# Optimization experiments

Measured on AMD Instinct MI355X. Metric: run time of the kernel, lower is better.

Reference implementation:

```python
import jax, jax.numpy as jnp
import numpy as np

N = 8192
D_IN = 512
D_OUT = 512


def setup_inputs() -> dict:
    key = jax.random.key(0)
    k1, k2, k3, k4 = jax.random.split(key, 4)
    x = jax.random.normal(k1, (N, D_IN), dtype=jnp.float32)
    adj = jax.random.uniform(k2, (N, N), dtype=jnp.float32)
    # nn.Linear params: weight (out, in), bias (out,)
    bound = 1.0 / np.sqrt(D_IN)
    W = jax.random.uniform(k3, (D_OUT, D_IN), minval=-bound, maxval=bound, dtype=jnp.float32)
    b = jax.random.uniform(k4, (D_OUT,), minval=-bound, maxval=bound, dtype=jnp.float32)
    return {"x": x, "adj": adj, "W": W, "b": b}


def reference(x, adj, W, b):
    # Symmetric normalization: D^-1/2 (A + I) D^-1/2.
    # Original uses diag-matmuls; broadcast scaling is the identical math
    # without the O(n^3) diagonal GEMMs.
    a = adj + jnp.eye(adj.shape[0], dtype=adj.dtype)
    d = jnp.sum(a, axis=1) ** -0.5  # (N,)
    a_norm = d[:, None] * a * d[None, :]
    support = a_norm @ x                      # (N, D_IN)
    out = support @ W.T + b                   # (N, D_OUT)
    out = jax.nn.relu(out)
    # dropout: identity in eval/reference mode
    return out
```

## Files before the change

kernel.cpp:

```cpp
#include <hip/hip_runtime.h>
#include <stdint.h>

typedef __bf16 bf16_t;
typedef __bf16 bf16x8 __attribute__((ext_vector_type(8)));
typedef __bf16 bf16x4v __attribute__((ext_vector_type(4)));
typedef float f32x4 __attribute__((ext_vector_type(4)));

#define AS_GLOBAL __attribute__((address_space(1)))
#define AS_LDS    __attribute__((address_space(3)))

static constexpr int NN   = 8192;
static constexpr int DIN  = 512;
static constexpr int DOUT = 512;
static constexpr int SPLITK = 4;

__device__ __forceinline__ void async_cp16(const bf16_t* g, bf16_t* l) {
  __builtin_amdgcn_global_load_lds((AS_GLOBAL unsigned int*)g,
                                   (AS_LDS unsigned int*)l, 16, 0, 0);
}

__global__ __launch_bounds__(256) void k_rowsum_convert(
    const float* __restrict__ adj, bf16_t* __restrict__ adjb,
    float* __restrict__ d) {
  const int row = blockIdx.x;
  const int t = threadIdx.x;
  const float4* rf4 = (const float4*)(adj + (size_t)row * NN);
  bf16_t* outp = adjb + (size_t)row * NN;
  float sum = 0.f;
#pragma unroll
  for (int c = 0; c < 8; ++c) {
    int f4i = c * 256 + t;
    float4 a = rf4[f4i];
    sum += a.x + a.y + a.z + a.w;
    bf16x4v o;
    o[0] = (bf16_t)a.x; o[1] = (bf16_t)a.y; o[2] = (bf16_t)a.z; o[3] = (bf16_t)a.w;
    *(bf16x4v*)(outp + f4i * 4) = o;
  }
#pragma unroll
  for (int off = 32; off > 0; off >>= 1) sum += __shfl_down(sum, off);
  __shared__ float red[4];
  if ((t & 63) == 0) red[t >> 6] = sum;
  __syncthreads();
  if (t == 0) {
    float s = red[0] + red[1] + red[2] + red[3] + 1.0f;
    d[row] = rsqrtf(s);
  }
}

__global__ __launch_bounds__(256) void k_make_xsT(
    const float* __restrict__ x, const float* __restrict__ d,
    bf16_t* __restrict__ xsT) {
  __shared__ bf16_t T[64][72];
  const int t = threadIdx.x;
  const int k0 = blockIdx.x * 64, j0 = blockIdx.y * 64;
#pragma unroll
  for (int it = 0; it < 4; ++it) {
    int idx = it * 256 + t;
    int r = idx >> 4, c = idx & 15;
    float4 v = *(const float4*)(x + (size_t)(k0 + r) * DIN + j0 + c * 4);
    float s = d[k0 + r];
    T[r][c * 4 + 0] = (bf16_t)(v.x * s);
    T[r][c * 4 + 1] = (bf16_t)(v.y * s);
    T[r][c * 4 + 2] = (bf16_t)(v.z * s);
    T[r][c * 4 + 3] = (bf16_t)(v.w * s);
  }
  __syncthreads();
#pragma unroll
  for (int it = 0; it < 2; ++it) {
    int idx = it * 256 + t;
    int j = idx >> 3, kb = idx & 7;
    bf16x8 o;
#pragma unroll
    for (int e = 0; e < 8; ++e) o[e] = T[kb * 8 + e][j];
    *(bf16x8*)(xsT + (size_t)(j0 + j) * NN + k0 + kb * 8) = o;
  }
}

__global__ __launch_bounds__(256) void k_convert_w(
    const float* __restrict__ W, bf16_t* __restrict__ Wb) {
  int idx = blockIdx.x * 256 + threadIdx.x;
  float4 v = *(const float4*)(W + (size_t)idx * 4);
  bf16x4v o;
  o[0] = (bf16_t)v.x; o[1] = (bf16_t)v.y; o[2] = (bf16_t)v.z; o[3] = (bf16_t)v.w;
  *(bf16x4v*)(Wb + (size_t)idx * 4) = o;
}

__device__ __forceinline__ void gemm_tile_128x128(
    const bf16_t* __restrict__ A, const bf16_t* __restrict__ B,
    int lda, int ldb, int m0, int n0, int kStart, int kEnd,
    bf16_t* As, bf16_t* Bs, f32x4 acc[4][4]) {
  const int t = threadIdx.x;
  const int lane = t & 63;
  const int wid = t >> 6;
  const int wm = wid >> 1, wn = wid & 1;
  const int lanelo = lane & 15, quad = lane >> 4;

  const int swz = (t & 7) ^ ((t >> 3) & 7);
  const bf16_t* gA = A + (size_t)(m0 + (t >> 3)) * lda + swz * 8 + kStart;
  const bf16_t* gB = B + (size_t)(n0 + (t >> 3)) * ldb + swz * 8 + kStart;
  bf16_t* lA = As + t * 8;
  bf16_t* lB = Bs + t * 8;

  const int xorc = lanelo & 7;

  for (int k0 = kStart; k0 < kEnd; k0 += 64) {
#pragma unroll
    for (int i = 0; i < 4; ++i) {
      async_cp16(gA + (size_t)(i * 32) * lda, lA + i * 2048);
      async_cp16(gB + (size_t)(i * 32) * ldb, lB + i * 2048);
    }
    gA += 64; gB += 64;
    __syncthreads();
#pragma unroll
    for (int kk = 0; kk < 2; ++kk) {
      const int pchunk = ((kk * 4 + quad) ^ xorc) * 8;
      bf16x8 av[4], bv[4];
#pragma unroll
      for (int f = 0; f < 4; ++f) {
        av[f] = *(const bf16x8*)(As + (wm * 64 + f * 16 + lanelo) * 64 + pchunk);
        bv[f] = *(const bf16x8*)(Bs + (wn * 64 + f * 16 + lanelo) * 64 + pchunk);
      }
#pragma unroll
      for (int fm = 0; fm < 4; ++fm)
#pragma unroll
        for (int fn = 0; fn < 4; ++fn)
          acc[fm][fn] = __builtin_amdgcn_mfma_f32_16x16x32_bf16(
              av[fm], bv[fn], acc[fm][fn], 0, 0, 0);
    }
    __syncthreads();
  }
}

__global__ __launch_bounds__(256) void k_gemm1(
    const bf16_t* __restrict__ adjb, const bf16_t* __restrict__ xsT,
    float* __restrict__ part) {
  __shared__ bf16_t As[128 * 64];
  __shared__ bf16_t Bs[128 * 64];
  f32x4 acc[4][4];
  const f32x4 fzero = {0.f, 0.f, 0.f, 0.f};
#pragma unroll
  for (int a = 0; a < 4; ++a)
#pragma unroll
    for (int b = 0; b < 4; ++b) acc[a][b] = fzero;

  const int m0 = blockIdx.x * 128, n0 = blockIdx.y * 128;
  const int kc = blockIdx.z;
  const int kChunk = NN / SPLITK;
  gemm_tile_128x128(adjb, xsT, NN, NN, m0, n0, kc * kChunk, (kc + 1) * kChunk,
                    As, Bs, acc);

  const int t = threadIdx.x;
  const int lane = t & 63, wid = t >> 6;
  const int wm = wid >> 1, wn = wid & 1;
  const int lanelo = lane & 15, quad = lane >> 4;
  float* outp = part + (size_t)kc * NN * DIN;
#pragma unroll
  for (int fm = 0; fm < 4; ++fm)
#pragma unroll
    for (int fn = 0; fn < 4; ++fn) {
      int gc = n0 + wn * 64 + fn * 16 + lanelo;
#pragma unroll
      for (int r = 0; r < 4; ++r) {
        int gr = m0 + wm * 64 + fm * 16 + quad * 4 + r;
        outp[(size_t)gr * DIN + gc] = acc[fm][fn][r];
      }
    }
}

__global__ __launch_bounds__(256) void k_combine(
    const float* __restrict__ part, const float* __restrict__ d,
    const float* __restrict__ x, bf16_t* __restrict__ supB) {
  int idx = blockIdx.x * 256 + threadIdx.x;
  int i = idx >> 7;
  float4 p = *(const float4*)(part + (size_t)idx * 4);
#pragma unroll
  for (int kc = 1; kc < SPLITK; ++kc) {
    float4 q = *(const float4*)(part + (size_t)kc * NN * DIN + (size_t)idx * 4);
    p.x += q.x; p.y += q.y; p.z += q.z; p.w += q.w;
  }
  float4 xv = *(const float4*)(x + (size_t)idx * 4);
  float di = d[i];
  float dii = di * di;
  bf16x4v o;
  o[0] = (bf16_t)(di * p.x + dii * xv.x);
  o[1] = (bf16_t)(di * p.y + dii * xv.y);
  o[2] = (bf16_t)(di * p.z + dii * xv.z);
  o[3] = (bf16_t)(di * p.w + dii * xv.w);
  *(bf16x4v*)(supB + (size_t)idx * 4) = o;
}

__global__ __launch_bounds__(256) void k_gemm2(
    const bf16_t* __restrict__ supB, const bf16_t* __restrict__ Wb,
    const float* __restrict__ bias, float* __restrict__ outp) {
  __shared__ bf16_t As[128 * 64];
  __shared__ bf16_t Bs[128 * 64];
  f32x4 acc[4][4];
  const f32x4 fzero = {0.f, 0.f, 0.f, 0.f};
#pragma unroll
  for (int a = 0; a < 4; ++a)
#pragma unroll
    for (int b = 0; b < 4; ++b) acc[a][b] = fzero;

  const int m0 = blockIdx.x * 128, n0 = blockIdx.y * 128;
  gemm_tile_128x128(supB, Wb, DIN, DIN, m0, n0, 0, DIN, As, Bs, acc);

  const int t = threadIdx.x;
  const int lane = t & 63, wid = t >> 6;
  const int wm = wid >> 1, wn = wid & 1;
  const int lanelo = lane & 15, quad = lane >> 4;
#pragma unroll
  for (int fn = 0; fn < 4; ++fn) {
    int gc = n0 + wn * 64 + fn * 16 + lanelo;
    float bb = bias[gc];
#pragma unroll
    for (int fm = 0; fm < 4; ++fm)
#pragma unroll
      for (int r = 0; r < 4; ++r) {
        int gr = m0 + wm * 64 + fm * 16 + quad * 4 + r;
        float v = acc[fm][fn][r] + bb;
        outp[(size_t)gr * DOUT + gc] = v > 0.f ? v : 0.f;
      }
  }
}

extern "C" void kernel_launch(void* const* d_in, const int* in_sizes, int n_in,
                              void* d_out, int out_size, void* d_ws, size_t ws_size,
                              hipStream_t stream) {
  const float* x   = (const float*)d_in[0];
  const float* adj = (const float*)d_in[1];
  const float* W   = (const float*)d_in[2];
  const float* b   = (const float*)d_in[3];
  float* out = (float*)d_out;

  char* ws = (char*)d_ws;
  bf16_t* adjb = (bf16_t*)(ws);
  float*  part = (float*)(ws + 134217728);
  size_t  off  = 134217728 + (size_t)SPLITK * NN * DIN * 4;
  bf16_t* xsT  = (bf16_t*)(ws + off);
  bf16_t* supB = (bf16_t*)(ws + off + 8388608);
  bf16_t* Wb   = (bf16_t*)(ws + off + 16777216);
  float*  dvec = (float*)(ws + off + 17301504);

  k_rowsum_convert<<<NN, 256, 0, stream>>>(adj, adjb, dvec);
  k_make_xsT<<<dim3(NN / 64, DIN / 64), 256, 0, stream>>>(x, dvec, xsT);
  k_convert_w<<<(DOUT * DIN) / 1024, 256, 0, stream>>>(W, Wb);
  k_gemm1<<<dim3(NN / 128, DIN / 128, SPLITK), 256, 0, stream>>>(adjb, xsT, part);
  k_combine<<<(NN * DIN) / 1024, 256, 0, stream>>>(part, dvec, x, supB);
  k_gemm2<<<dim3(NN / 128, DOUT / 128), 256, 0, stream>>>(supB, Wb, b, out);
}
```

Before: 532.7 us.

## Switch GEMMs to 32x32x16 MFMA and halve split-K for gemm1

Both GEMM kernels move from 16x16x32 bf16 MFMA tiles to 32x32x16 tiles. Each wave now holds a 2x2 grid of 32x32 accumulators, which changes the LDS fragment reads and the output index mapping. The larger instruction needs fewer LDS reads per FLOP. Split-K for the big adjacency GEMM also drops from 4 to 2, which halves the partial-sum traffic written by gemm1 and read by the combine kernel, but also halves the number of blocks in flight.

Result: faster. 518.3 us (-2.7%).

```diff
diff --git a/kernel.cpp b/kernel.cpp
--- a/kernel.cpp
+++ b/kernel.cpp
@@ -4,7 +4,7 @@
 typedef __bf16 bf16_t;
 typedef __bf16 bf16x8 __attribute__((ext_vector_type(8)));
 typedef __bf16 bf16x4v __attribute__((ext_vector_type(4)));
-typedef float f32x4 __attribute__((ext_vector_type(4)));
+typedef float f32x16 __attribute__((ext_vector_type(16)));
 
 #define AS_GLOBAL __attribute__((address_space(1)))
 #define AS_LDS    __attribute__((address_space(3)))
@@ -12,7 +12,7 @@
 static constexpr int NN   = 8192;
 static constexpr int DIN  = 512;
 static constexpr int DOUT = 512;
-static constexpr int SPLITK = 4;
+static constexpr int SPLITK = 2;
 
 __device__ __forceinline__ void async_cp16(const bf16_t* g, bf16_t* l) {
   __builtin_amdgcn_global_load_lds((AS_GLOBAL unsigned int*)g,
@@ -88,12 +88,12 @@
 __device__ __forceinline__ void gemm_tile_128x128(
     const bf16_t* __restrict__ A, const bf16_t* __restrict__ B,
     int lda, int ldb, int m0, int n0, int kStart, int kEnd,
-    bf16_t* As, bf16_t* Bs, f32x4 acc[4][4]) {
+    bf16_t* As, bf16_t* Bs, f32x16 acc[2][2]) {
   const int t = threadIdx.x;
   const int lane = t & 63;
   const int wid = t >> 6;
   const int wm = wid >> 1, wn = wid & 1;
-  const int lanelo = lane & 15, quad = lane >> 4;
+  const int l32 = lane & 31, half = lane >> 5;
 
   const int swz = (t & 7) ^ ((t >> 3) & 7);
   const bf16_t* gA = A + (size_t)(m0 + (t >> 3)) * lda + swz * 8 + kStart;
@@ -101,7 +101,7 @@
   bf16_t* lA = As + t * 8;
   bf16_t* lB = Bs + t * 8;
 
-  const int xorc = lanelo & 7;
+  const int xorc = lane & 7;
 
   for (int k0 = kStart; k0 < kEnd; k0 += 64) {
 #pragma unroll
@@ -112,19 +112,19 @@
     gA += 64; gB += 64;
     __syncthreads();
 #pragma unroll
-    for (int kk = 0; kk < 2; ++kk) {
-      const int pchunk = ((kk * 4 + quad) ^ xorc) * 8;
-      bf16x8 av[4], bv[4];
-#pragma unroll
-      for (int f = 0; f < 4; ++f) {
-        av[f] = *(const bf16x8*)(As + (wm * 64 + f * 16 + lanelo) * 64 + pchunk);
-        bv[f] = *(const bf16x8*)(Bs + (wn * 64 + f * 16 + lanelo) * 64 + pchunk);
+    for (int ks = 0; ks < 4; ++ks) {
+      const int pchunk = ((ks * 2 + half) ^ xorc) * 8;
+      bf16x8 av[2], bv[2];
+#pragma unroll
+      for (int f = 0; f < 2; ++f) {
+        av[f] = *(const bf16x8*)(As + (wm * 64 + f * 32 + l32) * 64 + pchunk);
+        bv[f] = *(const bf16x8*)(Bs + (wn * 64 + f * 32 + l32) * 64 + pchunk);
       }
 #pragma unroll
-      for (int fm = 0; fm < 4; ++fm)
-#pragma unroll
-        for (int fn = 0; fn < 4; ++fn)
-          acc[fm][fn] = __builtin_amdgcn_mfma_f32_16x16x32_bf16(
+      for (int fm = 0; fm < 2; ++fm)
+#pragma unroll
+        for (int fn = 0; fn < 2; ++fn)
+          acc[fm][fn] = __builtin_amdgcn_mfma_f32_32x32x16_bf16(
               av[fm], bv[fn], acc[fm][fn], 0, 0, 0);
     }
     __syncthreads();
@@ -136,12 +136,13 @@
     float* __restrict__ part) {
   __shared__ bf16_t As[128 * 64];
   __shared__ bf16_t Bs[128 * 64];
-  f32x4 acc[4][4];
-  const f32x4 fzero = {0.f, 0.f, 0.f, 0.f};
-#pragma unroll
-  for (int a = 0; a < 4; ++a)
-#pragma unroll
-    for (int b = 0; b < 4; ++b) acc[a][b] = fzero;
+  f32x16 acc[2][2];
+#pragma unroll
+  for (int a = 0; a < 2; ++a)
+#pragma unroll
+    for (int b = 0; b < 2; ++b)
+#pragma unroll
+      for (int r = 0; r < 16; ++r) acc[a][b][r] = 0.f;
 
   const int m0 = blockIdx.x * 128, n0 = blockIdx.y * 128;
   const int kc = blockIdx.z;
@@ -152,17 +153,17 @@
   const int t = threadIdx.x;
   const int lane = t & 63, wid = t >> 6;
   const int wm = wid >> 1, wn = wid & 1;
-  const int lanelo = lane & 15, quad = lane >> 4;
+  const int l32 = lane & 31, half = lane >> 5;
   float* outp = part + (size_t)kc * NN * DIN;
 #pragma unroll
-  for (int fm = 0; fm < 4; ++fm)
-#pragma unroll
-    for (int fn = 0; fn < 4; ++fn) {
-      int gc = n0 + wn * 64 + fn * 16 + lanelo;
-#pragma unroll
-      for (int r = 0; r < 4; ++r) {
-        int gr = m0 + wm * 64 + fm * 16 + quad * 4 + r;
-        outp[(size_t)gr * DIN + gc] = acc[fm][fn][r];
+  for (int fm = 0; fm < 2; ++fm)
+#pragma unroll
+    for (int fn = 0; fn < 2; ++fn) {
+      int gc = n0 + wn * 64 + fn * 32 + l32;
+#pragma unroll
+      for (int reg = 0; reg < 16; ++reg) {
+        int gr = m0 + wm * 64 + fm * 32 + (reg & 3) + 8 * (reg >> 2) + 4 * half;
+        outp[(size_t)gr * DIN + gc] = acc[fm][fn][reg];
       }
     }
 }
@@ -194,12 +195,13 @@
     const float* __restrict__ bias, float* __restrict__ outp) {
   __shared__ bf16_t As[128 * 64];
   __shared__ bf16_t Bs[128 * 64];
-  f32x4 acc[4][4];
-  const f32x4 fzero = {0.f, 0.f, 0.f, 0.f};
-#pragma unroll
-  for (int a = 0; a < 4; ++a)
-#pragma unroll
-    for (int b = 0; b < 4; ++b) acc[a][b] = fzero;
+  f32x16 acc[2][2];
+#pragma unroll
+  for (int a = 0; a < 2; ++a)
+#pragma unroll
+    for (int b = 0; b < 2; ++b)
+#pragma unroll
+      for (int r = 0; r < 16; ++r) acc[a][b][r] = 0.f;
 
   const int m0 = blockIdx.x * 128, n0 = blockIdx.y * 128;
   gemm_tile_128x128(supB, Wb, DIN, DIN, m0, n0, 0, DIN, As, Bs, acc);
@@ -207,17 +209,17 @@
   const int t = threadIdx.x;
   const int lane = t & 63, wid = t >> 6;
   const int wm = wid >> 1, wn = wid & 1;
-  const int lanelo = lane & 15, quad = lane >> 4;
-#pragma unroll
-  for (int fn = 0; fn < 4; ++fn) {
-    int gc = n0 + wn * 64 + fn * 16 + lanelo;
+  const int l32 = lane & 31, half = lane >> 5;
+#pragma unroll
+  for (int fn = 0; fn < 2; ++fn) {
+    int gc = n0 + wn * 64 + fn * 32 + l32;
     float bb = bias[gc];
 #pragma unroll
-    for (int fm = 0; fm < 4; ++fm)
-#pragma unroll
-      for (int r = 0; r < 4; ++r) {
-        int gr = m0 + wm * 64 + fm * 16 + quad * 4 + r;
-        float v = acc[fm][fn][r] + bb;
+    for (int fm = 0; fm < 2; ++fm)
+#pragma unroll
+      for (int reg = 0; reg < 16; ++reg) {
+        int gr = m0 + wm * 64 + fm * 32 + (reg & 3) + 8 * (reg >> 2) + 4 * half;
+        float v = acc[fm][fn][reg] + bb;
         outp[(size_t)gr * DOUT + gc] = v > 0.f ? v : 0.f;
       }
   }
```
